# Kernel optimization log

Measured on AMD Instinct MI355X. Metric: run time of the kernel, lower is better.

The kernel has to match this reference:

```python
import jax, jax.numpy as jnp
import numpy as np
import math

E, N, K, R = 1024, 16, 4, 64  # embed_dim, state_dim, d_conv, dt_rank=ceil(E/16)
B, L = 2, 2048


def setup_inputs() -> dict:
    key = jax.random.key(0)
    ks = jax.random.split(key, 8)
    gn = lambda k, sh, sc: jax.random.normal(k, sh, dtype=jnp.float32) * sc
    W_z = gn(ks[0], (E, E), E ** -0.5)                      # in_proj_z weight (no bias)
    W_params = gn(ks[1], (R + 2 * N, E), E ** -0.5)         # in_proj_params weight (no bias)
    conv_w = gn(ks[2], (E, 1, K), 0.5)                      # depthwise conv1d weight, no bias
    dt_std = R ** -0.5 * 0.1
    W_dt = jax.random.uniform(ks[3], (E, R), jnp.float32, -dt_std, dt_std)
    b_dt = jnp.full((E,), math.log(math.expm1(0.001)), dtype=jnp.float32)
    A_log = jnp.tile(jnp.log(jnp.arange(1, N + 1, dtype=jnp.float32))[None, :], (E, 1))
    D = jnp.ones((E,), dtype=jnp.float32)
    W_out = gn(ks[4], (E, E), E ** -0.5)
    x = jax.random.normal(ks[5], (B, L, E), dtype=jnp.float32)
    return dict(x=x, W_z=W_z, W_params=W_params, conv_w=conv_w, W_dt=W_dt,
                b_dt=b_dt, A_log=A_log, D=D, W_out=W_out)


def reference(x, W_z, W_params, conv_w, W_dt, b_dt, A_log, D, W_out):
    b, l, e = x.shape
    n = A_log.shape[1]
    r = W_dt.shape[1]
    k = conv_w.shape[-1]

    z = x @ W_z.T                                           # [B,L,E]
    params = x @ W_params.T                                 # [B,L,R+2N]
    dt_unproj = params[..., :r]
    # B_proj = params[..., r:r+n] is computed but UNUSED in the original forward
    C_proj = params[..., r + n:]                            # [B,L,N]
    dt = jax.nn.softplus(dt_unproj @ W_dt.T + b_dt)         # [B,L,E]

    # depthwise causal conv: torch pads K-1 both sides then slices [:L] == left-pad K-1
    xc = jax.lax.conv_general_dilated(
        x.transpose(0, 2, 1), conv_w, (1,), [(k - 1, 0)],
        dimension_numbers=('NCH', 'OIH', 'NCH'), feature_group_count=e)
    u = jax.nn.silu(xc.transpose(0, 2, 1))                  # [B,L,E]

    A = -jnp.exp(A_log)                                     # [E,N]
    A_tilde = jnp.exp(dt[..., None] * A[None, None])        # [B,L,E,N]
    B_tilde = jnp.where(jnp.abs(A)[None, None] < 1e-5,
                        dt[..., None],
                        (A_tilde - 1.0) / (A[None, None] + 1e-10))

    # recurrence (note t-1 indexing, faithful to original):
    # h_0 = B~[0]*u[0];  h_t = A~[t-1]*h_{t-1} + B~[t-1]*u[t-1]
    h0 = B_tilde[:, 0] * u[:, 0, :, None]                   # [B,E,N]

    def step(h, inp):
        a, bt, uu = inp
        h_new = a * h + bt * uu[..., None]
        return h_new, h_new

    xs = (A_tilde[:, :-1].transpose(1, 0, 2, 3),
          B_tilde[:, :-1].transpose(1, 0, 2, 3),
          u[:, :-1].transpose(1, 0, 2))
    _, hs = jax.lax.scan(step, h0, xs)                      # [L-1,B,E,N]
    h = jnp.concatenate([h0[None], hs], axis=0).transpose(1, 0, 2, 3)  # [B,L,E,N]

    y = jnp.einsum('bln,blen->ble', C_proj, h)
    y_ssm = y + u * D
    y_gated = y_ssm * jax.nn.silu(z)
    return y_gated @ W_out.T
```

## Files before the change

### kernel.cpp

```cpp
#include <hip/hip_runtime.h>
#include <math.h>

#define B_ 2
#define L_ 2048
#define E_ 1024
#define N_ 16
#define R_ 64
#define PWP 128
#define BL_ (B_*L_)

using bf16x8 = __attribute__((ext_vector_type(8))) short;
using f32x4  = __attribute__((ext_vector_type(4))) float;

__device__ __forceinline__ float softplusf(float x) {
    return fmaxf(x, 0.0f) + log1pf(expf(-fabsf(x)));
}
__device__ __forceinline__ float siluf(float x) {
    return x / (1.0f + expf(-x));
}
__device__ __forceinline__ ushort f2bf(float f) {
    unsigned u = __float_as_uint(f);
    return (ushort)((u + 0x7fffu + ((u >> 16) & 1u)) >> 16);
}
__device__ __forceinline__ float bf2f(ushort h) {
    return __uint_as_float(((unsigned)h) << 16);
}
__device__ __forceinline__ void gload16(const ushort* g, ushort* l) {
    __builtin_amdgcn_global_load_lds((const __attribute__((address_space(1))) void*)g,
                                     (__attribute__((address_space(3))) void*)l, 16, 0, 0);
}

__device__ __forceinline__ void split_body(const float* __restrict__ src, int spitch,
                                           int rows_src, ushort* __restrict__ dst,
                                           int K, int total4, int idx) {
    if (idx >= total4) return;
    const int Kq = K >> 2;
    const int r  = idx / Kq;
    const int c4 = (idx - r * Kq) << 2;
    float f[4] = {0.f, 0.f, 0.f, 0.f};
    if (r < rows_src)
        *reinterpret_cast<float4*>(f) = *reinterpret_cast<const float4*>(src + (size_t)r * spitch + c4);
    ushort h[4], lo[4];
#pragma unroll
    for (int q = 0; q < 4; ++q) {
        h[q]  = f2bf(f[q]);
        lo[q] = f2bf(f[q] - bf2f(h[q]));
    }
    ushort* d0 = dst + (size_t)r * 2 * K + c4;
    *reinterpret_cast<uint2*>(d0)     = make_uint2((uint)h[0]  | ((uint)h[1]  << 16), (uint)h[2]  | ((uint)h[3]  << 16));
    *reinterpret_cast<uint2*>(d0 + K) = make_uint2((uint)lo[0] | ((uint)lo[1] << 16), (uint)lo[2] | ((uint)lo[3] << 16));
}

__global__ __launch_bounds__(256)
void split_rm(const float* __restrict__ src, int spitch, int rows_src,
              ushort* __restrict__ dst, int K, int total4) {
    split_body(src, spitch, rows_src, dst, K, total4, blockIdx.x * 256 + threadIdx.x);
}

__global__ __launch_bounds__(256)
void split_w3(const float* __restrict__ Wz, const float* __restrict__ Wp,
              const float* __restrict__ Wdt, ushort* __restrict__ WzC,
              ushort* __restrict__ WpC, ushort* __restrict__ WdtC) {
    const int idx = blockIdx.x * 256 + threadIdx.x;
    if (blockIdx.y == 0)      split_body(Wz,  E_, E_,  WzC,  E_, E_ * E_ / 4, idx);
    else if (blockIdx.y == 1) split_body(Wp,  E_, 96,  WpC,  E_, 128 * E_ / 4, idx);
    else                      split_body(Wdt, R_, E_,  WdtC, R_, E_ * R_ / 4, idx);
}

__global__ __launch_bounds__(256)
void split_tr(const float* __restrict__ ygT, ushort* __restrict__ Ycat) {
    __shared__ float Ts[64][65];
    const int e0 = blockIdx.x * 64;
    const int l0 = blockIdx.y * 64;
    const int b  = blockIdx.z;
    const int tid = threadIdx.x;
    for (int idx = tid; idx < 64 * 64; idx += 256) {
        const int rr = idx >> 6, cc = idx & 63;
        Ts[rr][cc] = ygT[((size_t)(b * E_ + e0 + rr) << 11) + l0 + cc];
    }
    __syncthreads();
    for (int idx = tid; idx < 64 * 16; idx += 256) {
        const int rl = idx >> 4, g = idx & 15;
        ushort h[4], lo[4];
#pragma unroll
        for (int q = 0; q < 4; ++q) {
            const float f = Ts[g * 4 + q][rl];
            h[q]  = f2bf(f);
            lo[q] = f2bf(f - bf2f(h[q]));
        }
        ushort* d0 = Ycat + (size_t)(b * L_ + l0 + rl) * 2 * E_ + e0 + g * 4;
        *reinterpret_cast<uint2*>(d0)      = make_uint2((uint)h[0]  | ((uint)h[1]  << 16), (uint)h[2]  | ((uint)h[3]  << 16));
        *reinterpret_cast<uint2*>(d0 + E_) = make_uint2((uint)lo[0] | ((uint)lo[1] << 16), (uint)lo[2] | ((uint)lo[3] << 16));
    }
}

template<int BM, int BN, int BK, int MODE>
__global__ __launch_bounds__(256)
void mfma_gemm(const ushort* __restrict__ A, const ushort* __restrict__ Bm,
               const float* __restrict__ bias, ushort* __restrict__ P2,
               float* __restrict__ C, int Kd, int Ncols) {
    constexpr int WTM = BM / 2, WTN = BN / 2;
    constexpr int MI = WTM / 16, NJ = WTN / 16;
    constexpr int CPR = BK / 8;
    constexpr int KS  = BK / 32;
    constexpr int RPW = 64 / CPR;
    __shared__ ushort As[BM * BK];
    __shared__ ushort Bs[BN * BK];
    const int tid  = threadIdx.x;
    const int wave = tid >> 6, lane = tid & 63;
    const int m0 = blockIdx.x * BM, n0 = blockIdx.y * BN;
    const int wr = wave >> 1, wc = wave & 1;
    const int fr = lane & 15, fg = lane >> 4;
    const int kxor = (fr & 7) << 3;
    const int pK = 2 * Kd;

    f32x4 acc[MI][NJ];
#pragma unroll
    for (int i = 0; i < MI; ++i)
#pragma unroll
        for (int j = 0; j < NJ; ++j) { f32x4 z = {0.f, 0.f, 0.f, 0.f}; acc[i][j] = z; }

    const int lrow = lane / CPR;
    const int lc   = lane % CPR;

    const int KP = Kd / BK;
    for (int seg = 0; seg < 3; ++seg) {
        const int ao = (seg == 2) ? Kd : 0;
        const int bo = (seg == 1) ? Kd : 0;
        for (int tt = 0; tt < KP; ++tt) {
            const int ka = ao + tt * BK, kb = bo + tt * BK;
#pragma unroll
            for (int g = 0; g < BM / (4 * RPW); ++g) {
                const int srow = (wave * (BM / (4 * RPW)) + g) * RPW + lrow;
                const int sc = (lc & 8) | ((lc ^ (srow & 7)) & 7);
                gload16(A + (size_t)(m0 + srow) * pK + ka + sc * 8, As + srow * BK + lc * 8);
            }
#pragma unroll
            for (int g = 0; g < BN / (4 * RPW); ++g) {
                const int srow = (wave * (BN / (4 * RPW)) + g) * RPW + lrow;
                const int sc = (lc & 8) | ((lc ^ (srow & 7)) & 7);
                gload16(Bm + (size_t)(n0 + srow) * pK + kb + sc * 8, Bs + srow * BK + lc * 8);
            }
            __syncthreads();

#pragma unroll
            for (int ks = 0; ks < KS; ++ks) {
                bf16x8 av[MI], bv[NJ];
#pragma unroll
                for (int i = 0; i < MI; ++i) {
                    const int row = wr * WTM + i * 16 + fr;
                    av[i] = *reinterpret_cast<const bf16x8*>(&As[row * BK + ((ks * 32 + fg * 8) ^ kxor)]);
                }
#pragma unroll
                for (int j = 0; j < NJ; ++j) {
                    const int row = wc * WTN + j * 16 + fr;
                    bv[j] = *reinterpret_cast<const bf16x8*>(&Bs[row * BK + ((ks * 32 + fg * 8) ^ kxor)]);
                }
#pragma unroll
                for (int i = 0; i < MI; ++i)
#pragma unroll
                    for (int j = 0; j < NJ; ++j)
                        acc[i][j] = __builtin_amdgcn_mfma_f32_16x16x32_bf16(av[i], bv[j], acc[i][j], 0, 0, 0);
            }
            __syncthreads();
        }
    }

    if constexpr (MODE == 0) {
#pragma unroll
        for (int i = 0; i < MI; ++i) {
            const int m = m0 + wr * WTM + i * 16 + fg * 4;
#pragma unroll
            for (int j = 0; j < NJ; ++j) {
                const int n = n0 + wc * WTN + j * 16 + fr;
#pragma unroll
                for (int r = 0; r < 4; ++r)
                    C[(size_t)(m + r) * Ncols + n] = acc[i][j][r];
            }
        }
    } else if constexpr (MODE == 3) {
#pragma unroll
        for (int i = 0; i < MI; ++i) {
            const int m = m0 + wr * WTM + i * 16 + fg * 4;
#pragma unroll
            for (int j = 0; j < NJ; ++j) {
                const int n = n0 + wc * WTN + j * 16 + fr;
#pragma unroll
                for (int r = 0; r < 4; ++r) {
                    const float v = acc[i][j][r];
                    const int mm = m + r;
                    if (n < 64) {
                        const ushort hh = f2bf(v);
                        P2[(size_t)mm * 128 + n]      = hh;
                        P2[(size_t)mm * 128 + 64 + n] = f2bf(v - bf2f(hh));
                    } else if (n >= 80 && n < 96) {
                        C[(size_t)mm * Ncols + n] = v;
                    }
                }
            }
        }
    } else {
        const int b  = n0 >> 11;
        const int lb = n0 - (b << 11);
#pragma unroll
        for (int i = 0; i < MI; ++i) {
            const int e = m0 + wr * WTM + i * 16 + fg * 4;
#pragma unroll
            for (int r = 0; r < 4; ++r) {
                const float bia = (MODE == 2) ? bias[e + r] : 0.0f;
                float* row = C + ((size_t)(b * E_ + e + r) << 11) + lb;
#pragma unroll
                for (int j = 0; j < NJ; ++j) {
                    float v = acc[i][j][r];
                    if constexpr (MODE == 2) v = softplusf(v + bia);
                    row[wc * WTN + j * 16 + fr] = v;
                }
            }
        }
    }
}

__global__ __launch_bounds__(256)
void conv_split_kernel(const float* __restrict__ x, const float* __restrict__ cw,
                       float* __restrict__ uT, ushort* __restrict__ Xcat) {
    __shared__ float Xt[67][65];
    const int e0 = blockIdx.x * 64;
    const int l0 = blockIdx.y * 64;
    const int b  = blockIdx.z;
    const int tid = threadIdx.x;
    for (int idx = tid; idx < 67 * 64; idx += 256) {
        const int row = idx >> 6, col = idx & 63;
        const int gl = l0 - 3 + row;
        Xt[row][col] = (gl >= 0) ? x[((size_t)b * L_ + gl) * E_ + e0 + col] : 0.0f;
    }
    __syncthreads();
    const int lL = tid & 63;
    const int w  = tid >> 6;
    for (int ee = w; ee < 64; ee += 4) {
        const int e = e0 + ee;
        const float w0 = cw[e*4+0], w1 = cw[e*4+1], w2 = cw[e*4+2], w3 = cw[e*4+3];
        const float v = w0*Xt[lL][ee] + w1*Xt[lL+1][ee] + w2*Xt[lL+2][ee] + w3*Xt[lL+3][ee];
        uT[((size_t)b * E_ + e) * L_ + l0 + lL] = siluf(v);
    }
    for (int idx = tid; idx < 64 * 16; idx += 256) {
        const int rl = idx >> 4, g = idx & 15;
        ushort h[4], lo[4];
#pragma unroll
        for (int q = 0; q < 4; ++q) {
            const float f = Xt[3 + rl][g * 4 + q];
            h[q]  = f2bf(f);
            lo[q] = f2bf(f - bf2f(h[q]));
        }
        ushort* d0 = Xcat + (size_t)(b * L_ + l0 + rl) * 2 * E_ + e0 + g * 4;
        *reinterpret_cast<uint2*>(d0)      = make_uint2((uint)h[0]  | ((uint)h[1]  << 16), (uint)h[2]  | ((uint)h[3]  << 16));
        *reinterpret_cast<uint2*>(d0 + E_) = make_uint2((uint)lo[0] | ((uint)lo[1] << 16), (uint)lo[2] | ((uint)lo[3] << 16));
    }
}

__global__ __launch_bounds__(128)
void scan_kernel(const float* __restrict__ dtT, const float* __restrict__ uT,
                 const float* __restrict__ zT, const float* __restrict__ params,
                 const float* __restrict__ A_log, const float* __restrict__ Dp,
                 float* __restrict__ ygT) {
    __shared__ float sdt[64 * 33];
    __shared__ float su [64 * 33];
    __shared__ float wP1[N_], wL1[N_];
    const int c = blockIdx.x;
    const int b = c >> 10;
    const int e = c & (E_ - 1);
    const int tid  = threadIdx.x;
    const int wave = tid >> 6, lane = tid & 63;
    constexpr int CH = 16;
    constexpr float LOG2E = 1.44269504088896340736f;

    const float* dtp = dtT + ((size_t)b * E_ + e) * L_;
    const float* up  = uT  + ((size_t)b * E_ + e) * L_;
    const float* zp  = zT  + ((size_t)b * E_ + e) * L_;

#pragma unroll
    for (int it = 0; it < 4; ++it) {
        const int l = (it * 128 + tid) * 4;
        const int slot = ((l >> 5) * 33) + (l & 31);
        float4 vd = *reinterpret_cast<const float4*>(dtp + l);
        float4 vu = *reinterpret_cast<const float4*>(up  + l);
        sdt[slot] = vd.x; sdt[slot+1] = vd.y; sdt[slot+2] = vd.z; sdt[slot+3] = vd.w;
        su [slot] = vu.x; su [slot+1] = vu.y; su [slot+2] = vu.z; su [slot+3] = vu.w;
    }

    float An2[N_], rA[N_];
    unsigned selm = 0;
#pragma unroll
    for (int n = 0; n < N_; ++n) {
        const float A = -expf(A_log[e * N_ + n]);
        An2[n] = A * LOG2E;
        if (fabsf(A) < 1e-5f) selm |= (1u << n);
        rA[n] = 1.0f / (A + 1e-10f);
    }
    const float Dv = Dp[e];
    __syncthreads();

    const int base = (tid >> 1) * 33 + (tid & 1) * 16;
    const float d0 = sdt[0];
    const float u0 = su[0];

    float P[N_], h[N_];
#pragma unroll
    for (int n = 0; n < N_; ++n) { P[n] = 1.0f; h[n] = 0.0f; }
#pragma unroll 4
    for (int j = 0; j < CH; ++j) {
        const float d  = sdt[base + j];
        const float uu = su [base + j];
#pragma unroll
        for (int n = 0; n < N_; ++n) {
            const float at = __builtin_amdgcn_exp2f(d * An2[n]);
            const float bt = ((selm >> n) & 1u) ? d : (at - 1.0f) * rA[n];
            h[n] = fmaf(at, h[n], bt * uu);
            P[n] *= at;
        }
    }

#pragma unroll
    for (int off = 1; off < 64; off <<= 1) {
#pragma unroll
        for (int n = 0; n < N_; ++n) {
            const float Pp = __shfl_up(P[n], off);
            const float Lp = __shfl_up(h[n], off);
            if (lane >= off) {
                h[n] = fmaf(P[n], Lp, h[n]);
                P[n] *= Pp;
            }
        }
    }

    if (wave == 0 && lane == 63) {
#pragma unroll
        for (int n = 0; n < N_; ++n) { wP1[n] = P[n]; wL1[n] = h[n]; }
    }
    float cP[N_], cL[N_];
#pragma unroll
    for (int n = 0; n < N_; ++n) {
        cP[n] = __shfl_up(P[n], 1);
        cL[n] = __shfl_up(h[n], 1);
    }
    __syncthreads();

#pragma unroll
    for (int n = 0; n < N_; ++n) {
        const float pl = (lane == 0) ? 1.0f : cP[n];
        const float ll = (lane == 0) ? 0.0f : cL[n];
        float fP, fL;
        if (wave == 0) { fP = pl; fL = ll; }
        else           { fP = pl * wP1[n]; fL = fmaf(pl, wL1[n], ll); }
        const float at0 = __builtin_amdgcn_exp2f(d0 * An2[n]);
        const float bt0 = ((selm >> n) & 1u) ? d0 : (at0 - 1.0f) * rA[n];
        const float g0  = bt0 * u0;
        h[n] = fmaf(fP, g0, fL);
    }

    const float* crow = params + (size_t)b * L_ * PWP + 80;
    const int l0 = tid * CH;
    float4 pc0, pc1, pc2, pc3;
    {
        const float4* Cp4 = reinterpret_cast<const float4*>(crow + (size_t)l0 * PWP);
        pc0 = Cp4[0]; pc1 = Cp4[1]; pc2 = Cp4[2]; pc3 = Cp4[3];
    }
    float pz = zp[l0];
#pragma unroll
    for (int j = 0; j < CH; ++j) {
        float4 nc0, nc1, nc2, nc3; float nz = 0.0f;
        if (j < CH - 1) {
            const float4* Np = reinterpret_cast<const float4*>(crow + (size_t)(l0 + j + 1) * PWP);
            nc0 = Np[0]; nc1 = Np[1]; nc2 = Np[2]; nc3 = Np[3];
            nz = zp[l0 + j + 1];
        }
        const float d  = sdt[base + j];
        const float uu = su [base + j];
        float y = 0.0f;
        y = fmaf(pc0.x, h[0],  y); y = fmaf(pc0.y, h[1],  y);
        y = fmaf(pc0.z, h[2],  y); y = fmaf(pc0.w, h[3],  y);
        y = fmaf(pc1.x, h[4],  y); y = fmaf(pc1.y, h[5],  y);
        y = fmaf(pc1.z, h[6],  y); y = fmaf(pc1.w, h[7],  y);
        y = fmaf(pc2.x, h[8],  y); y = fmaf(pc2.y, h[9],  y);
        y = fmaf(pc2.z, h[10], y); y = fmaf(pc2.w, h[11], y);
        y = fmaf(pc3.x, h[12], y); y = fmaf(pc3.y, h[13], y);
        y = fmaf(pc3.z, h[14], y); y = fmaf(pc3.w, h[15], y);
        const float outv = (y + uu * Dv) * siluf(pz);
        if (j < CH - 1) {
#pragma unroll
            for (int n = 0; n < N_; ++n) {
                const float at = __builtin_amdgcn_exp2f(d * An2[n]);
                const float bt = ((selm >> n) & 1u) ? d : (at - 1.0f) * rA[n];
                h[n] = fmaf(at, h[n], bt * uu);
            }
        }
        sdt[base + j] = outv;
        pc0 = nc0; pc1 = nc1; pc2 = nc2; pc3 = nc3; pz = nz;
    }
    __syncthreads();

    float* yp = ygT + ((size_t)b * E_ + e) * L_;
#pragma unroll
    for (int it = 0; it < 4; ++it) {
        const int l = (it * 128 + tid) * 4;
        const int slot = ((l >> 5) * 33) + (l & 31);
        float4 o;
        o.x = sdt[slot]; o.y = sdt[slot+1]; o.z = sdt[slot+2]; o.w = sdt[slot+3];
        *reinterpret_cast<float4*>(yp + l) = o;
    }
}

extern "C" void kernel_launch(void* const* d_in, const int* in_sizes, int n_in,
                              void* d_out, int out_size, void* d_ws, size_t ws_size,
                              hipStream_t stream) {
    const float* x     = (const float*)d_in[0];
    const float* W_z   = (const float*)d_in[1];
    const float* W_p   = (const float*)d_in[2];
    const float* cw    = (const float*)d_in[3];
    const float* W_dt  = (const float*)d_in[4];
    const float* b_dt  = (const float*)d_in[5];
    const float* A_log = (const float*)d_in[6];
    const float* Dp    = (const float*)d_in[7];
    const float* W_out = (const float*)d_in[8];
    float* out = (float*)d_out;

    char* w = (char*)d_ws;
    ushort* Xcat   = (ushort*)(w);
    ushort* Wzcat  = (ushort*)(w + 16777216);
    ushort* Wpcat  = (ushort*)(w + 20971520);
    ushort* Wdtcat = (ushort*)(w + 21495808);
    ushort* Pcat   = (ushort*)(w + 21757952);
    float*  params = (float*)(w + 22806528);
    float*  zT     = (float*)(w + 24903680);
    float*  dtT    = (float*)(w + 41680896);
    float*  uT     = (float*)(w + 58458112);
    float*  ygT    = (float*)(w + 75235328);
    ushort* Ycat   = Xcat;
    ushort* Wocat  = Wzcat;

    conv_split_kernel<<<dim3(E_ / 64, L_ / 64, B_), 256, 0, stream>>>(x, cw, uT, Xcat);
    split_w3<<<dim3(1024, 3), 256, 0, stream>>>(W_z, W_p, W_dt, Wzcat, Wpcat, Wdtcat);
    mfma_gemm<128,64,128,1><<<dim3(E_ / 128, BL_ / 64), 256, 0, stream>>>(
        Wzcat, Xcat, nullptr, nullptr, zT, E_, 0);
    mfma_gemm<64,64,128,3><<<dim3(BL_ / 64, 2), 256, 0, stream>>>(
        Xcat, Wpcat, nullptr, Pcat, params, E_, PWP);
    mfma_gemm<128,64,64,2><<<dim3(E_ / 128, BL_ / 64), 256, 0, stream>>>(
        Wdtcat, Pcat, b_dt, nullptr, dtT, R_, 0);
    scan_kernel<<<B_ * E_, 128, 0, stream>>>(dtT, uT, zT, params, A_log, Dp, ygT);
    split_tr<<<dim3(E_ / 64, L_ / 64, B_), 256, 0, stream>>>(ygT, Ycat);
    split_rm<<<1024, 256, 0, stream>>>(W_out, E_, E_, Wocat, E_, E_ * E_ / 4);
    mfma_gemm<128,64,128,0><<<dim3(BL_ / 128, E_ / 64), 256, 0, stream>>>(
        Ycat, Wocat, nullptr, nullptr, out, E_, E_);
}
```

Measured before the change: 294.6 us.

## Fuse z and params projections into one GEMM; single-wave scan with closed-form chunk decay

The z projection and the params projection become a single MFMA GEMM over a concatenated weight (rows 0-1023 for W_z, rows 1024+ for W_params). Its epilogue routes output tiles either to transposed zT or to the split-bf16 dt input and the C columns. The scan kernel drops to one 64-thread wave with 32-step chunks, which removes the cross-wave LDS combine and the barrier. The per-chunk decay product is now computed as exp2 of the summed dt instead of a running product of 16 multiplies per step. The trade-off is fewer scan threads per block, longer serial chunks, and a dependence on the concatenated weight layout being contiguous in the workspace.

New measurement: 274.5 us. 6.8% less time.

```diff
diff --git a/kernel.cpp b/kernel.cpp
--- a/kernel.cpp
+++ b/kernel.cpp
@@ -98,7 +98,7 @@
 __global__ __launch_bounds__(256)
 void mfma_gemm(const ushort* __restrict__ A, const ushort* __restrict__ Bm,
                const float* __restrict__ bias, ushort* __restrict__ P2,
-               float* __restrict__ C, int Kd, int Ncols) {
+               float* __restrict__ C2, float* __restrict__ C, int Kd, int Ncols) {
     constexpr int WTM = BM / 2, WTN = BN / 2;
     constexpr int MI = WTM / 16, NJ = WTN / 16;
     constexpr int CPR = BK / 8;
@@ -178,28 +178,7 @@
                     C[(size_t)(m + r) * Ncols + n] = acc[i][j][r];
             }
         }
-    } else if constexpr (MODE == 3) {
-#pragma unroll
-        for (int i = 0; i < MI; ++i) {
-            const int m = m0 + wr * WTM + i * 16 + fg * 4;
-#pragma unroll
-            for (int j = 0; j < NJ; ++j) {
-                const int n = n0 + wc * WTN + j * 16 + fr;
-#pragma unroll
-                for (int r = 0; r < 4; ++r) {
-                    const float v = acc[i][j][r];
-                    const int mm = m + r;
-                    if (n < 64) {
-                        const ushort hh = f2bf(v);
-                        P2[(size_t)mm * 128 + n]      = hh;
-                        P2[(size_t)mm * 128 + 64 + n] = f2bf(v - bf2f(hh));
-                    } else if (n >= 80 && n < 96) {
-                        C[(size_t)mm * Ncols + n] = v;
-                    }
-                }
-            }
-        }
-    } else {
+    } else if constexpr (MODE == 2) {
         const int b  = n0 >> 11;
         const int lb = n0 - (b << 11);
 #pragma unroll
@@ -207,13 +186,47 @@
             const int e = m0 + wr * WTM + i * 16 + fg * 4;
 #pragma unroll
             for (int r = 0; r < 4; ++r) {
-                const float bia = (MODE == 2) ? bias[e + r] : 0.0f;
+                const float bia = bias[e + r];
                 float* row = C + ((size_t)(b * E_ + e + r) << 11) + lb;
 #pragma unroll
+                for (int j = 0; j < NJ; ++j)
+                    row[wc * WTN + j * 16 + fr] = softplusf(acc[i][j][r] + bia);
+            }
+        }
+    } else {
+        if (m0 < 1024) {
+            const int b  = n0 >> 11;
+            const int lb = n0 - (b << 11);
+#pragma unroll
+            for (int i = 0; i < MI; ++i) {
+                const int e = m0 + wr * WTM + i * 16 + fg * 4;
+#pragma unroll
+                for (int r = 0; r < 4; ++r) {
+                    float* row = C + ((size_t)(b * E_ + e + r) << 11) + lb;
+#pragma unroll
+                    for (int j = 0; j < NJ; ++j)
+                        row[wc * WTN + j * 16 + fr] = acc[i][j][r];
+                }
+            }
+        } else {
+#pragma unroll
+            for (int i = 0; i < MI; ++i) {
+                const int cb = m0 - 1024 + wr * WTM + i * 16 + fg * 4;
+#pragma unroll
                 for (int j = 0; j < NJ; ++j) {
-                    float v = acc[i][j][r];
-                    if constexpr (MODE == 2) v = softplusf(v + bia);
-                    row[wc * WTN + j * 16 + fr] = v;
+                    const int bl = n0 + wc * WTN + j * 16 + fr;
+#pragma unroll
+                    for (int r = 0; r < 4; ++r) {
+                        const float v = acc[i][j][r];
+                        const int cix = cb + r;
+                        if (cix < 64) {
+                            const ushort hh = f2bf(v);
+                            P2[(size_t)bl * 128 + cix]      = hh;
+                            P2[(size_t)bl * 128 + 64 + cix] = f2bf(v - bf2f(hh));
+                        } else if (cix >= 80 && cix < 96) {
+                            C2[(size_t)bl * PWP + cix] = v;
+                        }
+                    }
                 }
             }
         }
@@ -257,20 +270,18 @@
     }
 }
 
-__global__ __launch_bounds__(128)
+__global__ __launch_bounds__(64)
 void scan_kernel(const float* __restrict__ dtT, const float* __restrict__ uT,
                  const float* __restrict__ zT, const float* __restrict__ params,
                  const float* __restrict__ A_log, const float* __restrict__ Dp,
                  float* __restrict__ ygT) {
     __shared__ float sdt[64 * 33];
     __shared__ float su [64 * 33];
-    __shared__ float wP1[N_], wL1[N_];
     const int c = blockIdx.x;
     const int b = c >> 10;
     const int e = c & (E_ - 1);
-    const int tid  = threadIdx.x;
-    const int wave = tid >> 6, lane = tid & 63;
-    constexpr int CH = 16;
+    const int lane = threadIdx.x;
+    constexpr int CH = L_ / 64;
     constexpr float LOG2E = 1.44269504088896340736f;
 
     const float* dtp = dtT + ((size_t)b * E_ + e) * L_;
@@ -278,8 +289,8 @@
     const float* zp  = zT  + ((size_t)b * E_ + e) * L_;
 
 #pragma unroll
-    for (int it = 0; it < 4; ++it) {
-        const int l = (it * 128 + tid) * 4;
+    for (int it = 0; it < 8; ++it) {
+        const int l = (it * 64 + lane) * 4;
         const int slot = ((l >> 5) * 33) + (l & 31);
         float4 vd = *reinterpret_cast<const float4*>(dtp + l);
         float4 vu = *reinterpret_cast<const float4*>(up  + l);
@@ -299,25 +310,29 @@
     const float Dv = Dp[e];
     __syncthreads();
 
-    const int base = (tid >> 1) * 33 + (tid & 1) * 16;
+    const int base = lane * 33;
     const float d0 = sdt[0];
     const float u0 = su[0];
 
-    float P[N_], h[N_];
-#pragma unroll
-    for (int n = 0; n < N_; ++n) { P[n] = 1.0f; h[n] = 0.0f; }
+    float h[N_];
+    float dsum = 0.0f;
+#pragma unroll
+    for (int n = 0; n < N_; ++n) h[n] = 0.0f;
 #pragma unroll 4
     for (int j = 0; j < CH; ++j) {
         const float d  = sdt[base + j];
         const float uu = su [base + j];
+        dsum += d;
 #pragma unroll
         for (int n = 0; n < N_; ++n) {
             const float at = __builtin_amdgcn_exp2f(d * An2[n]);
             const float bt = ((selm >> n) & 1u) ? d : (at - 1.0f) * rA[n];
             h[n] = fmaf(at, h[n], bt * uu);
-            P[n] *= at;
-        }
-    }
+        }
+    }
+    float P[N_];
+#pragma unroll
+    for (int n = 0; n < N_; ++n) P[n] = __builtin_amdgcn_exp2f(dsum * An2[n]);
 
 #pragma unroll
     for (int off = 1; off < 64; off <<= 1) {
@@ -332,40 +347,30 @@
         }
     }
 
-    if (wave == 0 && lane == 63) {
-#pragma unroll
-        for (int n = 0; n < N_; ++n) { wP1[n] = P[n]; wL1[n] = h[n]; }
-    }
     float cP[N_], cL[N_];
 #pragma unroll
     for (int n = 0; n < N_; ++n) {
         cP[n] = __shfl_up(P[n], 1);
         cL[n] = __shfl_up(h[n], 1);
     }
-    __syncthreads();
 
 #pragma unroll
     for (int n = 0; n < N_; ++n) {
-        const float pl = (lane == 0) ? 1.0f : cP[n];
-        const float ll = (lane == 0) ? 0.0f : cL[n];
-        float fP, fL;
-        if (wave == 0) { fP = pl; fL = ll; }
-        else           { fP = pl * wP1[n]; fL = fmaf(pl, wL1[n], ll); }
         const float at0 = __builtin_amdgcn_exp2f(d0 * An2[n]);
         const float bt0 = ((selm >> n) & 1u) ? d0 : (at0 - 1.0f) * rA[n];
-        const float g0  = bt0 * u0;
-        h[n] = fmaf(fP, g0, fL);
+        const float g0 = bt0 * u0;
+        h[n] = (lane == 0) ? g0 : fmaf(cP[n], g0, cL[n]);
     }
 
     const float* crow = params + (size_t)b * L_ * PWP + 80;
-    const int l0 = tid * CH;
+    const int l0 = lane * CH;
     float4 pc0, pc1, pc2, pc3;
     {
         const float4* Cp4 = reinterpret_cast<const float4*>(crow + (size_t)l0 * PWP);
         pc0 = Cp4[0]; pc1 = Cp4[1]; pc2 = Cp4[2]; pc3 = Cp4[3];
     }
     float pz = zp[l0];
-#pragma unroll
+#pragma unroll 4
     for (int j = 0; j < CH; ++j) {
         float4 nc0, nc1, nc2, nc3; float nz = 0.0f;
         if (j < CH - 1) {
@@ -400,8 +405,8 @@
 
     float* yp = ygT + ((size_t)b * E_ + e) * L_;
 #pragma unroll
-    for (int it = 0; it < 4; ++it) {
-        const int l = (it * 128 + tid) * 4;
+    for (int it = 0; it < 8; ++it) {
+        const int l = (it * 64 + lane) * 4;
         const int slot = ((l >> 5) * 33) + (l & 31);
         float4 o;
         o.x = sdt[slot]; o.y = sdt[slot+1]; o.z = sdt[slot+2]; o.w = sdt[slot+3];
@@ -425,7 +430,7 @@
 
     char* w = (char*)d_ws;
     ushort* Xcat   = (ushort*)(w);
-    ushort* Wzcat  = (ushort*)(w + 16777216);
+    ushort* Wzpcat = (ushort*)(w + 16777216);
     ushort* Wpcat  = (ushort*)(w + 20971520);
     ushort* Wdtcat = (ushort*)(w + 21495808);
     ushort* Pcat   = (ushort*)(w + 21757952);
@@ -435,19 +440,17 @@
     float*  uT     = (float*)(w + 58458112);
     float*  ygT    = (float*)(w + 75235328);
     ushort* Ycat   = Xcat;
-    ushort* Wocat  = Wzcat;
+    ushort* Wocat  = Wzpcat;
 
     conv_split_kernel<<<dim3(E_ / 64, L_ / 64, B_), 256, 0, stream>>>(x, cw, uT, Xcat);
-    split_w3<<<dim3(1024, 3), 256, 0, stream>>>(W_z, W_p, W_dt, Wzcat, Wpcat, Wdtcat);
-    mfma_gemm<128,64,128,1><<<dim3(E_ / 128, BL_ / 64), 256, 0, stream>>>(
-        Wzcat, Xcat, nullptr, nullptr, zT, E_, 0);
-    mfma_gemm<64,64,128,3><<<dim3(BL_ / 64, 2), 256, 0, stream>>>(
-        Xcat, Wpcat, nullptr, Pcat, params, E_, PWP);
+    split_w3<<<dim3(1024, 3), 256, 0, stream>>>(W_z, W_p, W_dt, Wzpcat, Wpcat, Wdtcat);
+    mfma_gemm<128,64,128,4><<<dim3(1152 / 128, BL_ / 64), 256, 0, stream>>>(
+        Wzpcat, Xcat, nullptr, Pcat, params, zT, E_, 0);
     mfma_gemm<128,64,64,2><<<dim3(E_ / 128, BL_ / 64), 256, 0, stream>>>(
-        Wdtcat, Pcat, b_dt, nullptr, dtT, R_, 0);
-    scan_kernel<<<B_ * E_, 128, 0, stream>>>(dtT, uT, zT, params, A_log, Dp, ygT);
+        Wdtcat, Pcat, b_dt, nullptr, nullptr, dtT, R_, 0);
+    scan_kernel<<<B_ * E_, 64, 0, stream>>>(dtT, uT, zT, params, A_log, Dp, ygT);
     split_tr<<<dim3(E_ / 64, L_ / 64, B_), 256, 0, stream>>>(ygT, Ycat);
     split_rm<<<1024, 256, 0, stream>>>(W_out, E_, E_, Wocat, E_, E_ * E_ / 4);
     mfma_gemm<128,64,128,0><<<dim3(BL_ / 128, E_ / 64), 256, 0, stream>>>(
-        Ycat, Wocat, nullptr, nullptr, out, E_, E_);
-}
+        Ycat, Wocat, nullptr, nullptr, nullptr, out, E_, E_);
+}
```
